# Performance work log

Measured on AMD Instinct MI355X. Metric: run time of the kernel, lower is better.

The kernel has to match this reference:

```python
import jax, jax.numpy as jnp
import numpy as np

B, S, EMBED = 32, 2048, 256
N_QUBITS, N_QLAYERS = 8, 2
DIM = 2 ** N_QUBITS


def setup_inputs() -> dict:
    key = jax.random.key(0)
    k = jax.random.split(key, 6)
    x = jax.random.normal(k[0], (B, S, EMBED), jnp.float32)
    lim1 = 1.0 / np.sqrt(EMBED)
    W1 = jax.random.uniform(k[1], (N_QUBITS, EMBED), jnp.float32, -lim1, lim1)
    b1 = jax.random.uniform(k[2], (N_QUBITS,), jnp.float32, -lim1, lim1)
    # TorchLayer default init for BasicEntanglerLayers: uniform in [0, 2*pi)
    qw = jax.random.uniform(k[3], (N_QLAYERS, N_QUBITS), jnp.float32, 0.0, 2.0 * np.pi)
    lim2 = 1.0 / np.sqrt(N_QUBITS)
    W2 = jax.random.uniform(k[4], (EMBED, N_QUBITS), jnp.float32, -lim2, lim2)
    b2 = jax.random.uniform(k[5], (EMBED,), jnp.float32, -lim2, lim2)
    return {"x": x, "W1": W1, "b1": b1, "qw": qw, "W2": W2, "b2": b2}


def _rx(state, q, theta):
    # Apply RX(theta) on wire q (wire 0 = most significant bit).
    # state: [N, DIM] complex64; theta: scalar or [N]
    N = state.shape[0]
    a = 2 ** q
    b = DIM // (2 * a)
    s = state.reshape(N, a, 2, b)
    half = jnp.asarray(theta) * 0.5
    c = jnp.cos(half).reshape(-1, 1, 1)
    js = 1j * jnp.sin(half).reshape(-1, 1, 1)
    s0 = s[:, :, 0, :]
    s1 = s[:, :, 1, :]
    return jnp.stack([c * s0 - js * s1, c * s1 - js * s0], axis=2).reshape(N, DIM)


def _cnot(state, ctrl, tgt):
    # CNOT(ctrl -> tgt) on the batched statevector.
    s = state.reshape((-1,) + (2,) * N_QUBITS)
    ac, at = ctrl + 1, tgt + 1
    s0 = jax.lax.index_in_dim(s, 0, ac, keepdims=True)
    s1 = jax.lax.index_in_dim(s, 1, ac, keepdims=True)
    s1 = jnp.flip(s1, axis=at)  # X on target where control = 1
    return jnp.concatenate([s0, s1], axis=ac).reshape(state.shape)


def _circuit(angles, qw):
    # AngleEmbedding (RX) + BasicEntanglerLayers (RX + CNOT ring) + PauliZ expvals.
    # angles: [N, N_QUBITS] float; qw: [N_QLAYERS, N_QUBITS]
    N = angles.shape[0]
    state = jnp.zeros((N, DIM), jnp.complex64).at[:, 0].set(1.0)
    for q in range(N_QUBITS):
        state = _rx(state, q, angles[:, q])
    for l in range(N_QLAYERS):
        for q in range(N_QUBITS):
            state = _rx(state, q, qw[l, q])
        if N_QUBITS == 2:
            state = _cnot(state, 0, 1)
        elif N_QUBITS > 2:
            for q in range(N_QUBITS):
                state = _cnot(state, q, (q + 1) % N_QUBITS)
    probs = state.real ** 2 + state.imag ** 2  # [N, DIM]
    zs = []
    for q in range(N_QUBITS):
        p = probs.reshape(N, 2 ** q, 2, -1).sum(axis=(1, 3))  # [N, 2]
        zs.append(p[:, 0] - p[:, 1])
    return jnp.stack(zs, axis=1)  # [N, N_QUBITS]


def reference(x, W1, b1, qw, W2, b2):
    Bx, Sx, E = x.shape
    h = jnp.einsum('bse,qe->bsq', x, W1) + b1          # linear1 -> angles
    z = _circuit(h.reshape(-1, N_QUBITS), qw)          # batched over all tokens
    z = z.reshape(Bx, Sx, N_QUBITS).astype(x.dtype)
    return jnp.einsum('bsq,eq->bse', z, W2) + b2       # linear2
```

## Files before the change

kernel.cpp:

```cpp
#include <hip/hip_runtime.h>

#define EMBED 256

typedef _Float16 h2v __attribute__((ext_vector_type(2)));
typedef float f4v __attribute__((ext_vector_type(4)));

__device__ inline float rfl(float v) {
    return __uint_as_float(__builtin_amdgcn_readfirstlane(__float_as_uint(v)));
}
template<int CTRL>
__device__ inline float dppf(float v) {
    return __int_as_float(__builtin_amdgcn_mov_dpp(__float_as_int(v), CTRL, 0xf, 0xf, true));
}
__device__ inline float2 unpk2(int u) {
    h2v h = __builtin_bit_cast(h2v, u);
    return make_float2((float)h.x, (float)h.y);
}
__device__ inline int pk2(float a, float b) {
    return __builtin_bit_cast(int, __builtin_amdgcn_cvt_pkrtz(a, b));
}
__device__ inline void lds_fence() {
    asm volatile("s_waitcnt lgkmcnt(0)" ::: "memory");
}
__device__ inline void nt_store4(float* p, float a, float b, float c, float d) {
    f4v v = {a, b, c, d};
    __builtin_nontemporal_store(v, (f4v*)p);
}

constexpr unsigned MQ[8] = {0x03,0x06,0x0C,0x18,0x30,0x60,0xC0,0x83};
constexpr unsigned TQ[8] = {0xAB,0xFD,0xFA,0xF5,0xEA,0xD5,0xAA,0x55};
constexpr unsigned AQ[8] = {0xFE,0x03,0x07,0x0F,0x1F,0x3F,0x7F,0xFF};

constexpr int popc8(unsigned x) {
    int c = 0;
    for (int i = 0; i < 8; ++i) c += (x >> i) & 1;
    return c;
}
struct Term { int q; unsigned S; unsigned M; float sgn; };
struct TermTab { Term t[64]; int n; };
constexpr TermTab make_terms() {
    TermTab tt{};
    int n = 0;
    for (int q = 0; q < 8; ++q)
        for (unsigned S = 0; S < 256; ++S) {
            if ((S & ~AQ[q]) != 0) continue;
            unsigned M = 0;
            for (int j = 0; j < 8; ++j) if ((S >> j) & 1) M ^= MQ[j];
            if ((M & ~TQ[q]) != 0) continue;
            const int tot = popc8(S) + popc8(M);
            tt.t[n].q = q; tt.t[n].S = S; tt.t[n].M = M;
            tt.t[n].sgn = ((tot >> 1) & 1) ? -1.0f : 1.0f;
            ++n;
        }
    tt.n = n;
    return tt;
}
constexpr TermTab TT = make_terms();
static_assert(TT.n == 60, "term count");

__global__ __launch_bounds__(256) void fused_kernel(
    const float* __restrict__ x,
    const float* __restrict__ W1,
    const float* __restrict__ b1,
    const float* __restrict__ qw,
    const float* __restrict__ W2,
    const float* __restrict__ b2,
    float* __restrict__ out)
{
    const int tid  = threadIdx.x;
    const int lane = tid & 63;
    const int w    = tid >> 6;
    const int wid  = blockIdx.x * 4 + w;

    __shared__ alignas(16) int   hcs[4][64];
    __shared__ alignas(16) float zf[4][64];

    float4 w1c[8];
#pragma unroll
    for (int q = 0; q < 8; ++q)
        w1c[q] = *(const float4*)(W1 + q * EMBED + 4 * lane);
    const int aq = (lane >> 1) & 7;
    const float b1f = b1[aq] + qw[aq];

    float qc[8], qs[8];
#pragma unroll
    for (int j = 0; j < 8; ++j) {
        const float ph = qw[8 + j];
        qc[j] = rfl(__cosf(ph));
        qs[j] = rfl(__sinf(ph));
    }

    const bool s0 = lane & 1, s1 = lane & 2, s2 = lane & 4, s3 = lane & 8;

#pragma unroll
    for (int step = 0; step < 4; ++step) {
        const int p = wid * 4 + step;
        const float4 x0 = *(const float4*)(x + (size_t)p * 512 + 4 * lane);
        const float4 x1 = *(const float4*)(x + (size_t)p * 512 + 256 + 4 * lane);

        float vv[16];
#pragma unroll
        for (int q = 0; q < 8; ++q) {
            vv[2*q]   = x0.x*w1c[q].x + x0.y*w1c[q].y + x0.z*w1c[q].z + x0.w*w1c[q].w;
            vv[2*q+1] = x1.x*w1c[q].x + x1.y*w1c[q].y + x1.z*w1c[q].z + x1.w*w1c[q].w;
        }
#pragma unroll
        for (int i = 0; i < 8; ++i) {
            float a = vv[2*i], b = vv[2*i+1];
            float keep = s0 ? b : a, send = s0 ? a : b;
            vv[i] = keep + dppf<0xB1>(send);
        }
#pragma unroll
        for (int i = 0; i < 4; ++i) {
            float a = vv[2*i], b = vv[2*i+1];
            float keep = s1 ? b : a, send = s1 ? a : b;
            vv[i] = keep + dppf<0x4E>(send);
        }
#pragma unroll
        for (int i = 0; i < 2; ++i) {
            float a = vv[2*i], b = vv[2*i+1];
            float keep = s2 ? b : a, send = s2 ? a : b;
            vv[i] = keep + __shfl_xor(send, 4, 64);
        }
        {
            float a = vv[0], b = vv[1];
            float keep = s3 ? b : a, send = s3 ? a : b;
            vv[0] = keep + __shfl_xor(send, 8, 64);
        }
        float r = vv[0];
        r += __shfl_xor(r, 16, 64);
        r += __shfl_xor(r, 32, 64);

        const float th = r + b1f;
        const int pk = pk2(__cosf(th), __sinf(th));
        if (lane < 16)
            hcs[w][(2 * step + (lane & 1)) * 8 + (lane >> 1)] = pk;
    }
    lds_fence();

    const int sl = lane >> 3;
    const int q  = lane & 7;
    const int4 ua = *(const int4*)&hcs[w][sl * 8];
    const int4 ub = *(const int4*)&hcs[w][sl * 8 + 4];
    float u[8], v[8];
#define UNPK(U, Q) do { float2 f = unpk2(U); u[Q] = f.x; v[Q] = f.y; } while (0)
    UNPK(ua.x, 0); UNPK(ua.y, 1); UNPK(ua.z, 2); UNPK(ua.w, 3);
    UNPK(ub.x, 4); UNPK(ub.y, 5); UNPK(ub.z, 6); UNPK(ub.w, 7);
#undef UNPK

    float acc = 0.0f, psum = 0.0f;
#pragma unroll
    for (int t = 0; t < 60; ++t) {
        const int qt = TT.t[t].q;
        const unsigned S = TT.t[t].S, M = TT.t[t].M;
        float c = TT.t[t].sgn;
#pragma unroll
        for (int j = 0; j < 8; ++j)
            if ((AQ[qt] >> j) & 1) c *= ((S >> j) & 1) ? qs[j] : qc[j];
#pragma unroll
        for (int i = 0; i < 8; ++i)
            if ((TQ[qt] >> i) & 1) c *= ((M >> i) & 1) ? v[i] : u[i];
        psum += c;
        const bool qend = (t == 59) || (TT.t[t + 1].q != qt);
        if (qend) { acc += (q == qt) ? psum : 0.0f; psum = 0.0f; }
    }
    zf[w][lane] = acc;
    lds_fence();

    float4 w2f[8];
#pragma unroll
    for (int j = 0; j < 8; ++j)
        w2f[j] = *(const float4*)(W2 + (size_t)lane * 32 + 4 * j);
    const float4 b2c = *(const float4*)(b2 + 4 * lane);

    float* orow = out + (size_t)(wid * 8) * EMBED + 4 * lane;
#pragma unroll
    for (int r = 0; r < 8; ++r) {
        const float4 za = *(const float4*)&zf[w][r * 8];
        const float4 zb = *(const float4*)&zf[w][r * 8 + 4];
        const float zq[8] = {za.x, za.y, za.z, za.w, zb.x, zb.y, zb.z, zb.w};
        float o0 = b2c.x, o1 = b2c.y, o2 = b2c.z, o3 = b2c.w;
#pragma unroll
        for (int k = 0; k < 8; ++k) {
            const float* f0 = (const float*)&w2f[0 + (k >> 2)];
            const float* f1 = (const float*)&w2f[2 + (k >> 2)];
            const float* f2 = (const float*)&w2f[4 + (k >> 2)];
            const float* f3 = (const float*)&w2f[6 + (k >> 2)];
            o0 += zq[k] * f0[k & 3]; o1 += zq[k] * f1[k & 3];
            o2 += zq[k] * f2[k & 3]; o3 += zq[k] * f3[k & 3];
        }
        nt_store4(orow + (size_t)r * EMBED, o0, o1, o2, o3);
    }
}

extern "C" void kernel_launch(void* const* d_in, const int* in_sizes, int n_in,
                              void* d_out, int out_size, void* d_ws, size_t ws_size,
                              hipStream_t stream) {
    const float* x  = (const float*)d_in[0];
    const float* W1 = (const float*)d_in[1];
    const float* b1 = (const float*)d_in[2];
    const float* qw = (const float*)d_in[3];
    const float* W2 = (const float*)d_in[4];
    const float* b2 = (const float*)d_in[5];
    float* out = (float*)d_out;

    hipLaunchKernelGGL(fused_kernel, dim3(2048), dim3(256), 0, stream,
                       x, W1, b1, qw, W2, b2, out);
}
```

Before: 27.54 us.

## Stage W1 in LDS and split per-wave work into two non-unrolled iterations

W1 is now loaded once per block into shared memory, duplicated in two copies, and read from LDS inside the matvec instead of being held as 32 registers per lane. The per-wave work of 8 tokens is split into two rolled iterations of 4 tokens each. Each iteration runs the circuit evaluation with only half the lanes producing useful output and writes 4 output rows. The aim is to lower register pressure and raise occupancy. In exchange it adds LDS traffic, a block-wide barrier, reloads of W2 in each iteration, and half-idle lanes in the 60-term circuit loop, which roughly doubles that compute.

Measured after the change: 37.35 us. +35.6%, slower.

```diff
diff --git a/kernel.cpp b/kernel.cpp
--- a/kernel.cpp
+++ b/kernel.cpp
@@ -1,6 +1,7 @@
 #include <hip/hip_runtime.h>
 
 #define EMBED 256
+#define ITERS 2
 
 typedef _Float16 h2v __attribute__((ext_vector_type(2)));
 typedef float f4v __attribute__((ext_vector_type(4)));
@@ -72,16 +73,22 @@
     const int w    = tid >> 6;
     const int wid  = blockIdx.x * 4 + w;
 
-    __shared__ alignas(16) int   hcs[4][64];
-    __shared__ alignas(16) float zf[4][64];
-
-    float4 w1c[8];
-#pragma unroll
-    for (int q = 0; q < 8; ++q)
-        w1c[q] = *(const float4*)(W1 + q * EMBED + 4 * lane);
+    __shared__ alignas(16) float w1lds[2][2048];
+    __shared__ alignas(16) int   hcs[4][32];
+    __shared__ alignas(16) float zf[4][32];
+
+    {
+        const float4* src = (const float4*)W1;
+        const float4 a = src[tid * 2];
+        const float4 b = src[tid * 2 + 1];
+        *(float4*)&w1lds[0][tid * 8]     = a;
+        *(float4*)&w1lds[0][tid * 8 + 4] = b;
+        *(float4*)&w1lds[1][tid * 8]     = a;
+        *(float4*)&w1lds[1][tid * 8 + 4] = b;
+    }
+
     const int aq = (lane >> 1) & 7;
     const float b1f = b1[aq] + qw[aq];
-
     float qc[8], qs[8];
 #pragma unroll
     for (int j = 0; j < 8; ++j) {
@@ -89,107 +96,112 @@
         qc[j] = rfl(__cosf(ph));
         qs[j] = rfl(__sinf(ph));
     }
-
     const bool s0 = lane & 1, s1 = lane & 2, s2 = lane & 4, s3 = lane & 8;
 
-#pragma unroll
-    for (int step = 0; step < 4; ++step) {
-        const int p = wid * 4 + step;
-        const float4 x0 = *(const float4*)(x + (size_t)p * 512 + 4 * lane);
-        const float4 x1 = *(const float4*)(x + (size_t)p * 512 + 256 + 4 * lane);
-
-        float vv[16];
-#pragma unroll
-        for (int q = 0; q < 8; ++q) {
-            vv[2*q]   = x0.x*w1c[q].x + x0.y*w1c[q].y + x0.z*w1c[q].z + x0.w*w1c[q].w;
-            vv[2*q+1] = x1.x*w1c[q].x + x1.y*w1c[q].y + x1.z*w1c[q].z + x1.w*w1c[q].w;
-        }
-#pragma unroll
-        for (int i = 0; i < 8; ++i) {
-            float a = vv[2*i], b = vv[2*i+1];
-            float keep = s0 ? b : a, send = s0 ? a : b;
-            vv[i] = keep + dppf<0xB1>(send);
-        }
-#pragma unroll
-        for (int i = 0; i < 4; ++i) {
-            float a = vv[2*i], b = vv[2*i+1];
-            float keep = s1 ? b : a, send = s1 ? a : b;
-            vv[i] = keep + dppf<0x4E>(send);
-        }
-#pragma unroll
-        for (int i = 0; i < 2; ++i) {
-            float a = vv[2*i], b = vv[2*i+1];
-            float keep = s2 ? b : a, send = s2 ? a : b;
-            vv[i] = keep + __shfl_xor(send, 4, 64);
-        }
-        {
-            float a = vv[0], b = vv[1];
-            float keep = s3 ? b : a, send = s3 ? a : b;
-            vv[0] = keep + __shfl_xor(send, 8, 64);
-        }
-        float r = vv[0];
-        r += __shfl_xor(r, 16, 64);
-        r += __shfl_xor(r, 32, 64);
-
-        const float th = r + b1f;
-        const int pk = pk2(__cosf(th), __sinf(th));
-        if (lane < 16)
-            hcs[w][(2 * step + (lane & 1)) * 8 + (lane >> 1)] = pk;
-    }
-    lds_fence();
-
-    const int sl = lane >> 3;
-    const int q  = lane & 7;
-    const int4 ua = *(const int4*)&hcs[w][sl * 8];
-    const int4 ub = *(const int4*)&hcs[w][sl * 8 + 4];
-    float u[8], v[8];
+    __syncthreads();
+
+#pragma unroll 1
+    for (int it = 0; it < ITERS; ++it) {
+#pragma unroll
+        for (int step = 0; step < 2; ++step) {
+            const int p = wid * 4 + it * 2 + step;
+            const float4 x0 = *(const float4*)(x + (size_t)p * 512 + 4 * lane);
+            const float4 x1 = *(const float4*)(x + (size_t)p * 512 + 256 + 4 * lane);
+
+            float vv[16];
+#pragma unroll
+            for (int q = 0; q < 8; ++q) {
+                const f4v wq = *(const f4v*)&w1lds[it][q * 256 + 4 * lane];
+                vv[2*q]   = x0.x*wq[0] + x0.y*wq[1] + x0.z*wq[2] + x0.w*wq[3];
+                vv[2*q+1] = x1.x*wq[0] + x1.y*wq[1] + x1.z*wq[2] + x1.w*wq[3];
+            }
+#pragma unroll
+            for (int i = 0; i < 8; ++i) {
+                float a = vv[2*i], b = vv[2*i+1];
+                float keep = s0 ? b : a, send = s0 ? a : b;
+                vv[i] = keep + dppf<0xB1>(send);
+            }
+#pragma unroll
+            for (int i = 0; i < 4; ++i) {
+                float a = vv[2*i], b = vv[2*i+1];
+                float keep = s1 ? b : a, send = s1 ? a : b;
+                vv[i] = keep + dppf<0x4E>(send);
+            }
+#pragma unroll
+            for (int i = 0; i < 2; ++i) {
+                float a = vv[2*i], b = vv[2*i+1];
+                float keep = s2 ? b : a, send = s2 ? a : b;
+                vv[i] = keep + __shfl_xor(send, 4, 64);
+            }
+            {
+                float a = vv[0], b = vv[1];
+                float keep = s3 ? b : a, send = s3 ? a : b;
+                vv[0] = keep + __shfl_xor(send, 8, 64);
+            }
+            float r = vv[0];
+            r += __shfl_xor(r, 16, 64);
+            r += __shfl_xor(r, 32, 64);
+
+            const float th = r + b1f;
+            const int pk = pk2(__cosf(th), __sinf(th));
+            if (lane < 16)
+                hcs[w][(2 * step + (lane & 1)) * 8 + (lane >> 1)] = pk;
+        }
+        lds_fence();
+
+        const int sl = (lane >> 3) & 3;
+        const int q  = lane & 7;
+        const int4 ua = *(const int4*)&hcs[w][sl * 8];
+        const int4 ub = *(const int4*)&hcs[w][sl * 8 + 4];
+        float u[8], v[8];
 #define UNPK(U, Q) do { float2 f = unpk2(U); u[Q] = f.x; v[Q] = f.y; } while (0)
-    UNPK(ua.x, 0); UNPK(ua.y, 1); UNPK(ua.z, 2); UNPK(ua.w, 3);
-    UNPK(ub.x, 4); UNPK(ub.y, 5); UNPK(ub.z, 6); UNPK(ub.w, 7);
+        UNPK(ua.x, 0); UNPK(ua.y, 1); UNPK(ua.z, 2); UNPK(ua.w, 3);
+        UNPK(ub.x, 4); UNPK(ub.y, 5); UNPK(ub.z, 6); UNPK(ub.w, 7);
 #undef UNPK
 
-    float acc = 0.0f, psum = 0.0f;
-#pragma unroll
-    for (int t = 0; t < 60; ++t) {
-        const int qt = TT.t[t].q;
-        const unsigned S = TT.t[t].S, M = TT.t[t].M;
-        float c = TT.t[t].sgn;
+        float acc = 0.0f, psum = 0.0f;
+#pragma unroll
+        for (int t = 0; t < 60; ++t) {
+            const int qt = TT.t[t].q;
+            const unsigned S = TT.t[t].S, M = TT.t[t].M;
+            float c = TT.t[t].sgn;
+#pragma unroll
+            for (int j = 0; j < 8; ++j)
+                if ((AQ[qt] >> j) & 1) c *= ((S >> j) & 1) ? qs[j] : qc[j];
+#pragma unroll
+            for (int i = 0; i < 8; ++i)
+                if ((TQ[qt] >> i) & 1) c *= ((M >> i) & 1) ? v[i] : u[i];
+            psum += c;
+            const bool qend = (t == 59) || (TT.t[t + 1].q != qt);
+            if (qend) { acc += (q == qt) ? psum : 0.0f; psum = 0.0f; }
+        }
+        if (lane < 32) zf[w][lane] = acc;
+        lds_fence();
+
+        float4 w2f[8];
 #pragma unroll
         for (int j = 0; j < 8; ++j)
-            if ((AQ[qt] >> j) & 1) c *= ((S >> j) & 1) ? qs[j] : qc[j];
-#pragma unroll
-        for (int i = 0; i < 8; ++i)
-            if ((TQ[qt] >> i) & 1) c *= ((M >> i) & 1) ? v[i] : u[i];
-        psum += c;
-        const bool qend = (t == 59) || (TT.t[t + 1].q != qt);
-        if (qend) { acc += (q == qt) ? psum : 0.0f; psum = 0.0f; }
-    }
-    zf[w][lane] = acc;
-    lds_fence();
-
-    float4 w2f[8];
-#pragma unroll
-    for (int j = 0; j < 8; ++j)
-        w2f[j] = *(const float4*)(W2 + (size_t)lane * 32 + 4 * j);
-    const float4 b2c = *(const float4*)(b2 + 4 * lane);
-
-    float* orow = out + (size_t)(wid * 8) * EMBED + 4 * lane;
-#pragma unroll
-    for (int r = 0; r < 8; ++r) {
-        const float4 za = *(const float4*)&zf[w][r * 8];
-        const float4 zb = *(const float4*)&zf[w][r * 8 + 4];
-        const float zq[8] = {za.x, za.y, za.z, za.w, zb.x, zb.y, zb.z, zb.w};
-        float o0 = b2c.x, o1 = b2c.y, o2 = b2c.z, o3 = b2c.w;
-#pragma unroll
-        for (int k = 0; k < 8; ++k) {
-            const float* f0 = (const float*)&w2f[0 + (k >> 2)];
-            const float* f1 = (const float*)&w2f[2 + (k >> 2)];
-            const float* f2 = (const float*)&w2f[4 + (k >> 2)];
-            const float* f3 = (const float*)&w2f[6 + (k >> 2)];
-            o0 += zq[k] * f0[k & 3]; o1 += zq[k] * f1[k & 3];
-            o2 += zq[k] * f2[k & 3]; o3 += zq[k] * f3[k & 3];
-        }
-        nt_store4(orow + (size_t)r * EMBED, o0, o1, o2, o3);
+            w2f[j] = *(const float4*)(W2 + (size_t)lane * 32 + 4 * j);
+        const float4 b2c = *(const float4*)(b2 + 4 * lane);
+
+        float* orow = out + (size_t)(wid * 8 + it * 4) * EMBED + 4 * lane;
+#pragma unroll
+        for (int r = 0; r < 4; ++r) {
+            const float4 za = *(const float4*)&zf[w][r * 8];
+            const float4 zb = *(const float4*)&zf[w][r * 8 + 4];
+            const float zq[8] = {za.x, za.y, za.z, za.w, zb.x, zb.y, zb.z, zb.w};
+            float o0 = b2c.x, o1 = b2c.y, o2 = b2c.z, o3 = b2c.w;
+#pragma unroll
+            for (int k = 0; k < 8; ++k) {
+                const float* f0 = (const float*)&w2f[0 + (k >> 2)];
+                const float* f1 = (const float*)&w2f[2 + (k >> 2)];
+                const float* f2 = (const float*)&w2f[4 + (k >> 2)];
+                const float* f3 = (const float*)&w2f[6 + (k >> 2)];
+                o0 += zq[k] * f0[k & 3]; o1 += zq[k] * f1[k & 3];
+                o2 += zq[k] * f2[k & 3]; o3 += zq[k] * f3[k & 3];
+            }
+            nt_store4(orow + (size_t)r * EMBED, o0, o1, o2, o3);
+        }
     }
 }
 
```
